# Optimization experiments

Measured on AMD Instinct MI355X. Metric: run time of the kernel, lower is better.

## Reference

```python
import jax, jax.numpy as jnp
import numpy as np

N_NODES = 50000
N_EDGES = 800000
IN_F = 64
D_ATT = 64
HEADS = 8
D_HEAD = D_ATT // HEADS  # 8


def segment_softmax(logits, seg, num_segments):
    # logits: [E, d]; seg: [E] int segment ids
    m = jax.ops.segment_max(logits, seg, num_segments=num_segments)  # [N, d]
    m = jnp.where(jnp.isfinite(m), m, 0.0)  # guard empty segments
    e = jnp.exp(logits - m[seg])
    s = jax.ops.segment_sum(e, seg, num_segments=num_segments)  # [N, d]
    return e / (s[seg] + 1e-16)


def setup_inputs() -> dict:
    key = jax.random.key(0)
    ks = jax.random.split(key, 8)
    x = jax.random.normal(ks[0], (N_NODES, IN_F), dtype=jnp.float32)
    edge = jax.random.randint(ks[1], (2, N_EDGES), 0, N_NODES, dtype=jnp.int32)
    sc = 1.0 / np.sqrt(IN_F).astype(np.float32)
    Wq = jax.random.normal(ks[2], (IN_F, D_ATT), dtype=jnp.float32) * sc
    Wk = jax.random.normal(ks[3], (IN_F, D_ATT), dtype=jnp.float32) * sc
    Wv = jax.random.normal(ks[4], (IN_F, D_ATT), dtype=jnp.float32) * sc
    bq = jnp.zeros((D_ATT,), jnp.float32)
    bk = jnp.zeros((D_ATT,), jnp.float32)
    bv = jnp.zeros((D_ATT,), jnp.float32)
    return {"x": x, "Wq": Wq, "bq": bq, "Wk": Wk, "bk": bk, "Wv": Wv, "bv": bv, "edge": edge}


def reference(x, Wq, bq, Wk, bk, Wv, bv, edge):
    # Linear projections then split heads: [N, H, D_HEAD]
    q = (x @ Wq + bq).reshape(-1, HEADS, D_HEAD)
    k = (x @ Wk + bk).reshape(-1, HEADS, D_HEAD)
    v = (x @ Wv + bv).reshape(-1, HEADS, D_HEAD)
    src = q[edge[0]]      # [E, H, D_HEAD]
    dst_k = k[edge[1]]    # [E, H, D_HEAD]
    # Faithful to source: sum over dim=1 (the HEAD axis) -> [E, D_HEAD]
    prods = jnp.sum(src * dst_k, axis=1) / np.float32(np.sqrt(D_HEAD))
    # segment softmax grouped by edge[attention_norm_idx] (= edge[1])
    attention = segment_softmax(prods, edge[1], N_NODES)
    return attention, v, prods
```

## Files before the change

kernel.cpp:

```cpp
#include <hip/hip_runtime.h>
#include <hip/hip_bf16.h>

#define N_NODES 50000
#define N_EDGES 800000

__global__ __launch_bounds__(256, 4)
void proj_kernel(const float* __restrict__ x,
                 const float* __restrict__ Wq, const float* __restrict__ bq,
                 const float* __restrict__ Wk, const float* __restrict__ bk,
                 const float* __restrict__ Wv, const float* __restrict__ bv,
                 float* __restrict__ Qt, float* __restrict__ Kt,
                 float* __restrict__ V)
{
    __shared__ float xs[64 * 64];
    const int tid  = threadIdx.x;
    const int c    = tid & 63;
    const int w    = tid >> 6;
    const int m    = blockIdx.y;
    const int row0 = blockIdx.x * 64;
    const int nrows = min(64, N_NODES - row0);

    const float* W = (m == 0) ? Wq : (m == 1) ? Wk : Wv;
    const float* b = (m == 0) ? bq : (m == 1) ? bk : bv;
    const int oc = (m == 2) ? c : ((c & 7) * 8 + (c >> 3));
    float* out = (m == 0) ? Qt : (m == 1) ? Kt : V;

    {
        const float4* xg  = (const float4*)(x + (size_t)row0 * 64);
        float4*       xs4 = (float4*)xs;
        const int nf4 = nrows * 16;
        for (int i = tid; i < nf4; i += 256) xs4[i] = xg[i];
    }
    __syncthreads();

    const float bc = b[c];
    const int r0 = w * 16;

    float acc[16];
#pragma unroll
    for (int i = 0; i < 16; ++i) acc[i] = bc;

    for (int jc = 0; jc < 4; ++jc) {
        float wr[16];
#pragma unroll
        for (int j = 0; j < 16; ++j) wr[j] = W[(jc * 16 + j) * 64 + c];
#pragma unroll
        for (int i = 0; i < 16; ++i) {
            const float4* xr = (const float4*)(xs + (r0 + i) * 64 + jc * 16);
#pragma unroll
            for (int j4 = 0; j4 < 4; ++j4) {
                const float4 xv = xr[j4];
                acc[i] += xv.x * wr[4 * j4 + 0];
                acc[i] += xv.y * wr[4 * j4 + 1];
                acc[i] += xv.z * wr[4 * j4 + 2];
                acc[i] += xv.w * wr[4 * j4 + 3];
            }
        }
    }

#pragma unroll
    for (int i = 0; i < 16; ++i) {
        const int r = r0 + i;
        if (r < nrows) out[(size_t)(row0 + r) * 64 + oc] = acc[i];
    }
}

__global__ __launch_bounds__(256)
void edge_kernel(const float* __restrict__ Qt, const float* __restrict__ Kt,
                 const int* __restrict__ edge,
                 float* __restrict__ prods, float* __restrict__ att,
                 float* __restrict__ ssum)
{
    const int gid = blockIdx.x * 256 + threadIdx.x;
    if (gid >= N_EDGES * 8) return;
    const int e = gid >> 3;
    const int d = gid & 7;
    const int e0 = edge[e];
    const int e1 = edge[N_EDGES + e];

    const float4* qr = (const float4*)(Qt + (size_t)e0 * 64 + d * 8);
    const float4* kr = (const float4*)(Kt + (size_t)e1 * 64 + d * 8);
    const float4 q0 = qr[0], q1 = qr[1];
    const float4 k0 = kr[0], k1 = kr[1];
    float s = q0.x * k0.x + q0.y * k0.y + q0.z * k0.z + q0.w * k0.w
            + q1.x * k1.x + q1.y * k1.y + q1.z * k1.z + q1.w * k1.w;

    const float p = s * 0.35355339059327373f;
    prods[gid] = p;
    const float ex = __expf(p);
    att[gid] = ex;
    atomicAdd(ssum + (size_t)e1 * 8 + d, ex);
}

__global__ __launch_bounds__(256)
void norm_kernel(const int* __restrict__ edge,
                 const float* __restrict__ ssum, float* __restrict__ att)
{
    const int gid = blockIdx.x * 256 + threadIdx.x;
    if (gid >= N_EDGES * 8) return;
    const int e = gid >> 3;
    const int d = gid & 7;
    const int e1 = edge[N_EDGES + e];
    att[gid] = att[gid] / (ssum[(size_t)e1 * 8 + d] + 1e-16f);
}

extern "C" void kernel_launch(void* const* d_in, const int* in_sizes, int n_in,
                              void* d_out, int out_size, void* d_ws, size_t ws_size,
                              hipStream_t stream)
{
    const float* x    = (const float*)d_in[0];
    const float* Wq   = (const float*)d_in[1];
    const float* bq   = (const float*)d_in[2];
    const float* Wk   = (const float*)d_in[3];
    const float* bk   = (const float*)d_in[4];
    const float* Wv   = (const float*)d_in[5];
    const float* bv   = (const float*)d_in[6];
    const int*   edge = (const int*)d_in[7];

    float* out   = (float*)d_out;
    float* att   = out;
    float* V     = out + 6400000;
    float* prods = out + 9600000;

    float* Qt   = (float*)d_ws;
    float* Kt   = Qt + 3200000;
    float* ssum = Kt + 3200000;

    hipMemsetAsync(ssum, 0, 400000 * sizeof(float), stream);

    dim3 pgrid((N_NODES + 63) / 64, 3);
    proj_kernel<<<pgrid, 256, 0, stream>>>(x, Wq, bq, Wk, bk, Wv, bv,
                                           Qt, Kt, V);

    const int nwork = N_EDGES * 8;
    edge_kernel<<<(nwork + 255) / 256, 256, 0, stream>>>(Qt, Kt, edge, prods,
                                                         att, ssum);
    norm_kernel<<<(nwork + 255) / 256, 256, 0, stream>>>(edge, ssum, att);
}
```

Before: 197.3 us.

## Store Q/K in bf16 and recompute exp in norm kernel instead of storing att

The projection kernel now writes Q and K as bf16, which halves the gathered bytes per edge in the edge kernel. The edge kernel no longer writes the unnormalized exp to att. The norm kernel recomputes exp from prods instead of reading att back. This cuts gather and write traffic in exchange for bf16 rounding error in the attention logits, and it adds a small bf16 store pattern with 2-byte scattered writes in the projection kernel.

```diff
diff --git a/kernel.cpp b/kernel.cpp
--- a/kernel.cpp
+++ b/kernel.cpp
@@ -4,12 +4,26 @@
 #define N_NODES 50000
 #define N_EDGES 800000
 
+typedef __attribute__((ext_vector_type(4))) unsigned int uint4v;
+
+static __device__ __forceinline__ float bfu_lo(unsigned int u) {
+    union { unsigned int u; float f; } v; v.u = u << 16; return v.f;
+}
+static __device__ __forceinline__ float bfu_hi(unsigned int u) {
+    union { unsigned int u; float f; } v; v.u = u & 0xffff0000u; return v.f;
+}
+static __device__ __forceinline__ unsigned short f2bf(float f) {
+    union { float f; unsigned int u; } v; v.f = f;
+    v.u += 0x7fffu + ((v.u >> 16) & 1u);
+    return (unsigned short)(v.u >> 16);
+}
+
 __global__ __launch_bounds__(256, 4)
 void proj_kernel(const float* __restrict__ x,
                  const float* __restrict__ Wq, const float* __restrict__ bq,
                  const float* __restrict__ Wk, const float* __restrict__ bk,
                  const float* __restrict__ Wv, const float* __restrict__ bv,
-                 float* __restrict__ Qt, float* __restrict__ Kt,
+                 unsigned short* __restrict__ Qb, unsigned short* __restrict__ Kb,
                  float* __restrict__ V)
 {
     __shared__ float xs[64 * 64];
@@ -23,7 +37,7 @@
     const float* W = (m == 0) ? Wq : (m == 1) ? Wk : Wv;
     const float* b = (m == 0) ? bq : (m == 1) ? bk : bv;
     const int oc = (m == 2) ? c : ((c & 7) * 8 + (c >> 3));
-    float* out = (m == 0) ? Qt : (m == 1) ? Kt : V;
+    unsigned short* outb = (m == 0) ? Qb : Kb;
 
     {
         const float4* xg  = (const float4*)(x + (size_t)row0 * 64);
@@ -61,15 +75,19 @@
 #pragma unroll
     for (int i = 0; i < 16; ++i) {
         const int r = r0 + i;
-        if (r < nrows) out[(size_t)(row0 + r) * 64 + oc] = acc[i];
+        if (r < nrows) {
+            const size_t o = (size_t)(row0 + r) * 64 + oc;
+            if (m == 2) V[o] = acc[i];
+            else        outb[o] = f2bf(acc[i]);
+        }
     }
 }
 
 __global__ __launch_bounds__(256)
-void edge_kernel(const float* __restrict__ Qt, const float* __restrict__ Kt,
+void edge_kernel(const unsigned short* __restrict__ Qb,
+                 const unsigned short* __restrict__ Kb,
                  const int* __restrict__ edge,
-                 float* __restrict__ prods, float* __restrict__ att,
-                 float* __restrict__ ssum)
+                 float* __restrict__ prods, float* __restrict__ ssum)
 {
     const int gid = blockIdx.x * 256 + threadIdx.x;
     if (gid >= N_EDGES * 8) return;
@@ -78,22 +96,23 @@
     const int e0 = edge[e];
     const int e1 = edge[N_EDGES + e];
 
-    const float4* qr = (const float4*)(Qt + (size_t)e0 * 64 + d * 8);
-    const float4* kr = (const float4*)(Kt + (size_t)e1 * 64 + d * 8);
-    const float4 q0 = qr[0], q1 = qr[1];
-    const float4 k0 = kr[0], k1 = kr[1];
-    float s = q0.x * k0.x + q0.y * k0.y + q0.z * k0.z + q0.w * k0.w
-            + q1.x * k1.x + q1.y * k1.y + q1.z * k1.z + q1.w * k1.w;
+    const uint4v qv = *(const uint4v*)(Qb + (size_t)e0 * 64 + d * 8);
+    const uint4v kv = *(const uint4v*)(Kb + (size_t)e1 * 64 + d * 8);
+    float s = 0.f;
+#pragma unroll
+    for (int i = 0; i < 4; ++i) {
+        s += bfu_lo(qv[i]) * bfu_lo(kv[i]);
+        s += bfu_hi(qv[i]) * bfu_hi(kv[i]);
+    }
 
     const float p = s * 0.35355339059327373f;
     prods[gid] = p;
-    const float ex = __expf(p);
-    att[gid] = ex;
-    atomicAdd(ssum + (size_t)e1 * 8 + d, ex);
+    atomicAdd(ssum + (size_t)e1 * 8 + d, __expf(p));
 }
 
 __global__ __launch_bounds__(256)
 void norm_kernel(const int* __restrict__ edge,
+                 const float* __restrict__ prods,
                  const float* __restrict__ ssum, float* __restrict__ att)
 {
     const int gid = blockIdx.x * 256 + threadIdx.x;
@@ -101,7 +120,8 @@
     const int e = gid >> 3;
     const int d = gid & 7;
     const int e1 = edge[N_EDGES + e];
-    att[gid] = att[gid] / (ssum[(size_t)e1 * 8 + d] + 1e-16f);
+    const float ex = __expf(prods[gid]);
+    att[gid] = ex / (ssum[(size_t)e1 * 8 + d] + 1e-16f);
 }
 
 extern "C" void kernel_launch(void* const* d_in, const int* in_sizes, int n_in,
@@ -122,18 +142,19 @@
     float* V     = out + 6400000;
     float* prods = out + 9600000;
 
-    float* Qt   = (float*)d_ws;
-    float* Kt   = Qt + 3200000;
-    float* ssum = Kt + 3200000;
+    unsigned short* Qb = (unsigned short*)d_ws;
+    unsigned short* Kb = Qb + 3200000;
+    float*          ssum = (float*)(Kb + 3200000);
 
     hipMemsetAsync(ssum, 0, 400000 * sizeof(float), stream);
 
     dim3 pgrid((N_NODES + 63) / 64, 3);
     proj_kernel<<<pgrid, 256, 0, stream>>>(x, Wq, bq, Wk, bk, Wv, bv,
-                                           Qt, Kt, V);
+                                           Qb, Kb, V);
 
     const int nwork = N_EDGES * 8;
-    edge_kernel<<<(nwork + 255) / 256, 256, 0, stream>>>(Qt, Kt, edge, prods,
-                                                         att, ssum);
-    norm_kernel<<<(nwork + 255) / 256, 256, 0, stream>>>(edge, ssum, att);
+    edge_kernel<<<(nwork + 255) / 256, 256, 0, stream>>>(Qb, Kb, edge, prods,
+                                                         ssum);
+    norm_kernel<<<(nwork + 255) / 256, 256, 0, stream>>>(edge, prods, ssum,
+                                                         att);
 }
```

Measured after the change: 185.9 us. 1.06x faster.
